# Performance work log

Hardware: AMD Instinct MI355X
Metric: run time of the kernel (lower is better)

The kernel has to match this reference:

```python
import jax, jax.numpy as jnp
import numpy as np

NUM_HEADS = 16
NUM_KV_GROUPS = 4
EPS = 1e-6


def _rms_norm(x, w):
    # normalize over last dim (head_dim)
    return x * jax.lax.rsqrt(jnp.mean(x * x, axis=-1, keepdims=True) + EPS) * w


def _rope_cos_sin(T, head_dim):
    half = head_dim // 2
    inv_freq = 1.0 / (10000.0 ** (jnp.arange(half, dtype=jnp.float32) / half))
    freqs = jnp.arange(T, dtype=jnp.float32)[:, None] * inv_freq[None, :]  # [T, half]
    cos = jnp.repeat(jnp.cos(freqs), 2, axis=-1)  # [T, head_dim]
    sin = jnp.repeat(jnp.sin(freqs), 2, axis=-1)
    return cos, sin


def _apply_rope(x, cos, sin):
    # x: [B, H, T, head_dim]; cos/sin broadcast over B,H
    x1 = x[..., ::2]
    x2 = x[..., 1::2]
    x_rot = jnp.stack([-x2, x1], axis=-1).reshape(x.shape)  # interleave (-x2, x1)
    return x * cos + x_rot * sin


def setup_inputs() -> dict:
    key = jax.random.key(0)
    ks = jax.random.split(key, 5)
    scale = lambda k, sh: jax.random.normal(k, sh, dtype=jnp.float32) * 0.02
    return {
        "x": jax.random.normal(ks[0], (4, 2048, 1024), dtype=jnp.float32),
        "Wq": scale(ks[1], (1024, 1024)),
        "Wk": scale(ks[2], (256, 1024)),
        "Wv": scale(ks[3], (256, 1024)),
        "Wo": scale(ks[4], (1024, 1024)),
        "qn_w": jnp.ones((64,), jnp.float32),
        "kn_w": jnp.ones((64,), jnp.float32),
    }


def reference(x, Wq, Wk, Wv, Wo, qn_w, kn_w):
    B, T, D = x.shape
    H, G = NUM_HEADS, NUM_KV_GROUPS
    hd = D // H

    # projections (torch Linear: y = x @ W.T), reshape to [B, heads, T, hd]
    q = (x @ Wq.T).reshape(B, T, H, hd).transpose(0, 2, 1, 3)
    k = (x @ Wk.T).reshape(B, T, G, hd).transpose(0, 2, 1, 3)
    v = (x @ Wv.T).reshape(B, T, G, hd).transpose(0, 2, 1, 3)

    # optional qk RMSNorm (qk_norm=True)
    q = _rms_norm(q, qn_w)
    k = _rms_norm(k, kn_w)

    # RoPE (position_offset = 0)
    cos, sin = _rope_cos_sin(T, hd)
    q = _apply_rope(q, cos, sin)
    k = _apply_rope(k, cos, sin)

    # GQA: expand kv heads to match query heads
    rep = H // G
    k = jnp.repeat(k, rep, axis=1)
    v = jnp.repeat(v, rep, axis=1)

    # causal SDPA
    scores = jnp.einsum('bhqd,bhkd->bhqk', q, k) / jnp.sqrt(jnp.float32(hd))
    causal = jnp.tril(jnp.ones((T, T), dtype=bool))
    scores = jnp.where(causal, scores, jnp.float32(-1e30))
    attn = jax.nn.softmax(scores, axis=-1)
    out = jnp.einsum('bhqk,bhkd->bhqd', attn, v)

    out = out.transpose(0, 2, 1, 3).reshape(B, T, D)
    return out @ Wo.T
```

## Files before the change

kernel.cpp:

```cpp
#include <hip/hip_runtime.h>

typedef unsigned short u16;
typedef __attribute__((ext_vector_type(8))) short bf16x8;
typedef __attribute__((ext_vector_type(4))) short bf16x4;
typedef __attribute__((ext_vector_type(4))) float f32x4;

#define GP(p) ((const __attribute__((address_space(1))) void*)(unsigned long long)(p))
#define LP(p) ((__attribute__((address_space(3))) void*)(unsigned int)(unsigned long long)(p))

#define QSCALE 0.180336879486998f

__device__ __forceinline__ u16 f2bf(float f) {
  union { float f; unsigned u; } v; v.f = f;
  unsigned r = v.u + 0x7fffu + ((v.u >> 16) & 1u);
  return (u16)(r >> 16);
}
__device__ __forceinline__ short f2bf_cvt(float f) {
  __bf16 b = (__bf16)f;
  return *reinterpret_cast<short*>(&b);
}

#if __has_builtin(__builtin_amdgcn_mfma_f32_16x16x16bf16_1k)
#define MFMA16(A, B, C) __builtin_amdgcn_mfma_f32_16x16x16bf16_1k((A), (B), (C), 0, 0, 0)
#elif __has_builtin(__builtin_amdgcn_mfma_f32_16x16x16_bf16)
#define MFMA16(A, B, C) __builtin_amdgcn_mfma_f32_16x16x16_bf16((A), (B), (C), 0, 0, 0)
#else
static __device__ __forceinline__ f32x4 mfma16_asm(bf16x4 a, bf16x4 b, f32x4 c) {
  asm volatile("v_mfma_f32_16x16x16_bf16 %0, %1, %2, %0" : "+v"(c) : "v"(a), "v"(b));
  return c;
}
#define MFMA16(A, B, C) mfma16_asm((A), (B), (C))
#endif

__global__ void prep_kernel(const float* __restrict__ x,
                            const float* __restrict__ Wq, const float* __restrict__ Wk,
                            const float* __restrict__ Wv, const float* __restrict__ Wo,
                            u16* __restrict__ xb, u16* __restrict__ Wcat,
                            u16* __restrict__ Wob,
                            float* __restrict__ ctab, float* __restrict__ stab) {
  const int bid = blockIdx.x, tid = threadIdx.x;
  if (bid < 2048) {
    for (int i = bid * 256 + tid; i < 2097152; i += 2048 * 256) {
      float4 v = reinterpret_cast<const float4*>(x)[i];
      reinterpret_cast<ushort4*>(xb)[i] =
          make_ushort4(f2bf(v.x), f2bf(v.y), f2bf(v.z), f2bf(v.w));
    }
  } else if (bid < 2688) {
    for (int i = (bid - 2048) * 256 + tid; i < 655360; i += 640 * 256) {
      const float* src; u16* dst; int off;
      if (i < 262144)      { src = Wq; dst = Wcat;           off = i; }
      else if (i < 327680) { src = Wk; dst = Wcat + 1048576; off = i - 262144; }
      else if (i < 393216) { src = Wv; dst = Wcat + 1310720; off = i - 327680; }
      else                 { src = Wo; dst = Wob;            off = i - 393216; }
      float4 v = reinterpret_cast<const float4*>(src)[off];
      reinterpret_cast<ushort4*>(dst)[off] =
          make_ushort4(f2bf(v.x), f2bf(v.y), f2bf(v.z), f2bf(v.w));
    }
  } else {
    int i = (bid - 2688) * 256 + tid;
    int t = i >> 5, f = i & 31;
    float inv = exp2f((float)f * (-13.287712379549449f / 32.0f));
    float ang = (float)t * inv;
    float sv, cv;
    sincosf(ang, &sv, &cv);
    ctab[i] = cv;
    stab[i] = sv;
  }
}

__launch_bounds__(256)
__global__ void gemm_qkv_kernel(const u16* __restrict__ A, const u16* __restrict__ W,
                                u16* __restrict__ qh, u16* __restrict__ kh,
                                u16* __restrict__ vt,
                                const float* __restrict__ qn_w, const float* __restrict__ kn_w,
                                const float* __restrict__ ctab, const float* __restrict__ stab) {
  __shared__ __align__(16) u16 As[2][128 * 64];
  __shared__ __align__(16) u16 Bs[2][128 * 64];
  const int tid = threadIdx.x;
  const int w = tid >> 6, l = tid & 63;
  const int lr = l & 15, lk = l >> 4;
  const int wr = w >> 1, wc = w & 1;
  const int m0 = blockIdx.x * 128, n0 = blockIdx.y * 128;
  const u16* ap[4];
  const u16* bp[4];
#pragma unroll
  for (int i = 0; i < 4; ++i) {
    int c = i * 256 + tid;
    ap[i] = A + (size_t)(m0 + (c >> 3)) * 1024 + (c & 7) * 8;
    bp[i] = W + (size_t)(n0 + (c >> 3)) * 1024 + (c & 7) * 8;
  }
  auto stage = [&](int buf) {
#pragma unroll
    for (int i = 0; i < 4; ++i) {
      __builtin_amdgcn_global_load_lds(GP(ap[i]),
          LP((char*)&As[0][0] + buf * 16384 + (i * 256 + (tid & ~63)) * 16), 16, 0, 0);
      __builtin_amdgcn_global_load_lds(GP(bp[i]),
          LP((char*)&Bs[0][0] + buf * 16384 + (i * 256 + (tid & ~63)) * 16), 16, 0, 0);
      ap[i] += 64; bp[i] += 64;
    }
  };
  f32x4 acc[4][4] = {};
  int cur = 0;
  stage(0);
  asm volatile("s_waitcnt vmcnt(0)" ::: "memory");
  __builtin_amdgcn_s_barrier();
  for (int k0 = 0; k0 < 1024; k0 += 64) {
    if (k0 < 960) stage(cur ^ 1);
    __builtin_amdgcn_s_setprio(1);
#pragma unroll
    for (int kk = 0; kk < 2; ++kk) {
      bf16x8 af[4], bfr[4];
#pragma unroll
      for (int fi = 0; fi < 4; ++fi)
        af[fi] = *reinterpret_cast<const bf16x8*>(
            &As[cur][(wr * 64 + fi * 16 + lr) * 64 + kk * 32 + lk * 8]);
#pragma unroll
      for (int fj = 0; fj < 4; ++fj)
        bfr[fj] = *reinterpret_cast<const bf16x8*>(
            &Bs[cur][(wc * 64 + fj * 16 + lr) * 64 + kk * 32 + lk * 8]);
#pragma unroll
      for (int fi = 0; fi < 4; ++fi)
#pragma unroll
        for (int fj = 0; fj < 4; ++fj)
          acc[fi][fj] = __builtin_amdgcn_mfma_f32_16x16x32_bf16(af[fi], bfr[fj], acc[fi][fj], 0, 0, 0);
    }
    __builtin_amdgcn_s_setprio(0);
    asm volatile("s_waitcnt vmcnt(0)" ::: "memory");
    __builtin_amdgcn_s_barrier();
    cur ^= 1;
  }
  const int ncol0 = n0 + wc * 64;
  if (ncol0 < 1280) {
    const bool isq = ncol0 < 1024;
    const float* wn = isq ? qn_w : kn_w;
    const float sc = isq ? QSCALE : 1.0f;
    float wv[4];
#pragma unroll
    for (int fj = 0; fj < 4; ++fj) wv[fj] = wn[fj * 16 + lr];
#pragma unroll
    for (int fi = 0; fi < 4; ++fi)
#pragma unroll
      for (int r = 0; r < 4; ++r) {
        float ss = 0.f;
#pragma unroll
        for (int fj = 0; fj < 4; ++fj) ss += acc[fi][fj][r] * acc[fi][fj][r];
        ss += __shfl_xor(ss, 1); ss += __shfl_xor(ss, 2);
        ss += __shfl_xor(ss, 4); ss += __shfl_xor(ss, 8);
        float rinv = rsqrtf(ss * (1.0f / 64.0f) + 1e-6f);
        int m = m0 + wr * 64 + fi * 16 + lk * 4 + r;
        int t = m & 2047, b = m >> 11;
#pragma unroll
        for (int fj = 0; fj < 4; ++fj) {
          float xn = acc[fi][fj][r] * rinv * wv[fj];
          float pr = __shfl_xor(xn, 1);
          float rot = (lr & 1) ? pr : -pr;
          int ci = t * 32 + fj * 8 + (lr >> 1);
          u16 outv = f2bf((xn * ctab[ci] + rot * stab[ci]) * sc);
          int n = ncol0 + fj * 16 + lr;
          if (isq) {
            int h = n >> 6, d = n & 63;
            qh[((size_t)((b * 16 + h) * 2048 + t)) * 64 + d] = outv;
          } else {
            int n2 = n - 1024, g = n2 >> 6, d = n2 & 63;
            kh[((size_t)((b * 4 + g) * 2048 + t)) * 64 + d] = outv;
          }
        }
      }
  } else {
#pragma unroll
    for (int fi = 0; fi < 4; ++fi)
#pragma unroll
      for (int fj = 0; fj < 4; ++fj) {
        int m = m0 + wr * 64 + fi * 16 + lk * 4;
        int b = m >> 11, t = m & 2047;
        int n2 = ncol0 + fj * 16 + lr - 1280;
        int g = n2 >> 6, d = n2 & 63;
        bf16x4 o;
#pragma unroll
        for (int r = 0; r < 4; ++r) o[r] = f2bf_cvt(acc[fi][fj][r]);
        *reinterpret_cast<bf16x4*>(&vt[((size_t)((b * 4 + g) * 64 + d)) * 2048 + t]) = o;
      }
  }
}

__launch_bounds__(512)
__global__ void attn_kernel(const u16* __restrict__ qh, const u16* __restrict__ kh,
                            const u16* __restrict__ vt, u16* __restrict__ ao) {
  __shared__ __align__(16) u16 Ks[2][64 * 64];
  __shared__ __align__(16) u16 Vts[2][64 * 64];
  const int tid = threadIdx.x, w = tid >> 6, l = tid & 63;
  const int lr = l & 15, lk = l >> 4;
  const int wq = w & 3, wh = w >> 2;
  const int D = blockIdx.x;
  const int j = D >> 3;
  const int p = j & 15, hp = (j >> 4) & 1;
  const int z = (D & 7) + 8 * (j >> 5);
  const int b = z >> 2, g = z & 3;
  const int h = g * 4 + hp * 2 + wh;
  const u16* Qh = qh + ((size_t)((b * 16 + h) * 2048)) * 64;
  const u16* Kb = kh + ((size_t)z * 2048) * 64;
  const u16* Vtb = vt + ((size_t)z * 64) * 2048;
  const int swz = (lr & 7) * 8;

  const int r0 = tid >> 3, s0 = ((tid & 7) ^ (r0 & 7)) * 8;
  char* kd = (char*)&Ks[0][0] + (tid & ~63) * 16;
  char* vd = (char*)&Vts[0][0] + (tid & ~63) * 16;
  const u16* kp; const u16* vp;

  auto stage = [&](int buf) {
    __builtin_amdgcn_global_load_lds(GP(kp), LP(kd + buf * 8192), 16, 0, 0);
    __builtin_amdgcn_global_load_lds(GP(vp), LP(vd + buf * 8192), 16, 0, 0);
    kp += 64 * 64; vp += 64;
  };

  const u16* kbase[2];
  kbase[0] = &Ks[0][lr * 64 + ((lk * 8) ^ swz)];
  kbase[1] = &Ks[0][lr * 64 + ((32 + lk * 8) ^ swz)];
  const u16* vbase[4];
#pragma unroll
  for (int fi = 0; fi < 4; ++fi)
    vbase[fi] = &Vts[0][lr * 64 + ((fi * 16 + lk * 4) ^ swz)];

  auto run_qtile = [&](int qt) {
    const int q0 = qt * 64;
    const u16* Qb = Qh + (size_t)(q0 + wq * 16) * 64;
    const bf16x8 qf0 = *reinterpret_cast<const bf16x8*>(&Qb[lr * 64 + lk * 8]);
    const bf16x8 qf1 = *reinterpret_cast<const bf16x8*>(&Qb[lr * 64 + 32 + lk * 8]);
    f32x4 oacc[4] = {};
    float lrow = 0.f;
    kp = Kb + r0 * 64 + s0;
    vp = Vtb + (size_t)r0 * 2048 + s0;
    stage(0);
    asm volatile("s_waitcnt vmcnt(0)" ::: "memory");
    __builtin_amdgcn_s_barrier();

    auto round = [&](int it, int buf) {
      if (it < qt) stage(buf ^ 1);
      f32x4 sacc[4] = {};
      __builtin_amdgcn_s_setprio(1);
#pragma unroll
      for (int kk = 0; kk < 2; ++kk) {
        bf16x8 qf = kk ? qf1 : qf0;
#pragma unroll
        for (int fi = 0; fi < 4; ++fi) {
          bf16x8 kf = *reinterpret_cast<const bf16x8*>(kbase[kk] + buf * 4096 + fi * 1024);
          sacc[fi] = __builtin_amdgcn_mfma_f32_16x16x32_bf16(kf, qf, sacc[fi], 0, 0, 0);
        }
      }
      __builtin_amdgcn_s_setprio(0);
      if (it == qt) {
        int qloc = wq * 16 + lr;
#pragma unroll
        for (int fi = 0; fi < 4; ++fi)
#pragma unroll
          for (int r = 0; r < 4; ++r)
            if (fi * 16 + lk * 4 + r > qloc) sacc[fi][r] = -1e30f;
      }
      bf16x4 pb[4];
#pragma unroll
      for (int fi = 0; fi < 4; ++fi)
#pragma unroll
        for (int r = 0; r < 4; ++r) {
          float pv = exp2f(sacc[fi][r]);
          lrow += pv;
          pb[fi][r] = f2bf_cvt(pv);
        }
      __builtin_amdgcn_s_setprio(1);
#pragma unroll
      for (int fi = 0; fi < 4; ++fi)
#pragma unroll
        for (int db = 0; db < 4; ++db) {
          bf16x4 vf = *reinterpret_cast<const bf16x4*>(vbase[fi] + buf * 4096 + db * 1024);
          oacc[db] = MFMA16(vf, pb[fi], oacc[db]);
        }
      __builtin_amdgcn_s_setprio(0);
      asm volatile("s_waitcnt vmcnt(0)" ::: "memory");
      __builtin_amdgcn_s_barrier();
    };

    const int nIt = qt + 1;
    for (int it = 0; it < nIt; it += 2) {
      round(it, 0);
      if (it + 1 < nIt) round(it + 1, 1);
    }

    float lsum = lrow;
    lsum += __shfl_xor(lsum, 16);
    lsum += __shfl_xor(lsum, 32);
    float inv = 1.0f / lsum;
#pragma unroll
    for (int db = 0; db < 4; ++db) {
      bf16x4 o;
#pragma unroll
      for (int r = 0; r < 4; ++r) o[r] = f2bf_cvt(oacc[db][r] * inv);
      *reinterpret_cast<bf16x4*>(
          &ao[((size_t)(b * 2048 + q0 + wq * 16 + lr)) * 1024 + h * 64 + db * 16 + lk * 4]) = o;
    }
  };
  run_qtile(31 - p);
  run_qtile(p);
}

__launch_bounds__(256)
__global__ void gemm_out_kernel(const u16* __restrict__ A, const u16* __restrict__ W,
                                float* __restrict__ out) {
  __shared__ __align__(16) u16 As[2][128 * 64];
  __shared__ __align__(16) u16 Bs[2][128 * 64];
  const int tid = threadIdx.x;
  const int w = tid >> 6, l = tid & 63;
  const int lr = l & 15, lk = l >> 4;
  const int wr = w >> 1, wc = w & 1;
  const int bid = blockIdx.x;
  const int m0 = (bid >> 3) * 128, n0 = (bid & 7) * 128;
  const u16* ap[4];
  const u16* bp[4];
#pragma unroll
  for (int i = 0; i < 4; ++i) {
    int c = i * 256 + tid;
    ap[i] = A + (size_t)(m0 + (c >> 3)) * 1024 + (c & 7) * 8;
    bp[i] = W + (size_t)(n0 + (c >> 3)) * 1024 + (c & 7) * 8;
  }
  auto stage = [&](int buf) {
#pragma unroll
    for (int i = 0; i < 4; ++i) {
      __builtin_amdgcn_global_load_lds(GP(ap[i]),
          LP((char*)&As[0][0] + buf * 16384 + (i * 256 + (tid & ~63)) * 16), 16, 0, 0);
      __builtin_amdgcn_global_load_lds(GP(bp[i]),
          LP((char*)&Bs[0][0] + buf * 16384 + (i * 256 + (tid & ~63)) * 16), 16, 0, 0);
      ap[i] += 64; bp[i] += 64;
    }
  };
  f32x4 acc[4][4] = {};
  int cur = 0;
  stage(0);
  asm volatile("s_waitcnt vmcnt(0)" ::: "memory");
  __builtin_amdgcn_s_barrier();
  for (int k0 = 0; k0 < 1024; k0 += 64) {
    if (k0 < 960) stage(cur ^ 1);
    __builtin_amdgcn_s_setprio(1);
#pragma unroll
    for (int kk = 0; kk < 2; ++kk) {
      bf16x8 af[4], bfr[4];
#pragma unroll
      for (int fi = 0; fi < 4; ++fi)
        af[fi] = *reinterpret_cast<const bf16x8*>(
            &As[cur][(wr * 64 + fi * 16 + lr) * 64 + kk * 32 + lk * 8]);
#pragma unroll
      for (int fj = 0; fj < 4; ++fj)
        bfr[fj] = *reinterpret_cast<const bf16x8*>(
            &Bs[cur][(wc * 64 + fj * 16 + lr) * 64 + kk * 32 + lk * 8]);
#pragma unroll
      for (int fi = 0; fi < 4; ++fi)
#pragma unroll
        for (int fj = 0; fj < 4; ++fj)
          acc[fi][fj] = __builtin_amdgcn_mfma_f32_16x16x32_bf16(af[fi], bfr[fj], acc[fi][fj], 0, 0, 0);
    }
    __builtin_amdgcn_s_setprio(0);
    asm volatile("s_waitcnt vmcnt(0)" ::: "memory");
    __builtin_amdgcn_s_barrier();
    cur ^= 1;
  }
#pragma unroll
  for (int fi = 0; fi < 4; ++fi)
#pragma unroll
    for (int fj = 0; fj < 4; ++fj)
#pragma unroll
      for (int r = 0; r < 4; ++r) {
        int m = m0 + wr * 64 + fi * 16 + lk * 4 + r;
        int n = n0 + wc * 64 + fj * 16 + lr;
        out[(size_t)m * 1024 + n] = acc[fi][fj][r];
      }
}

extern "C" void kernel_launch(void* const* d_in, const int* in_sizes, int n_in,
                              void* d_out, int out_size, void* d_ws, size_t ws_size,
                              hipStream_t stream) {
  const float* x  = (const float*)d_in[0];
  const float* Wq = (const float*)d_in[1];
  const float* Wk = (const float*)d_in[2];
  const float* Wv = (const float*)d_in[3];
  const float* Wo = (const float*)d_in[4];
  const float* qn = (const float*)d_in[5];
  const float* kn = (const float*)d_in[6];
  float* out = (float*)d_out;
  char* ws = (char*)d_ws;
  u16* xb   = (u16*)(ws);
  u16* Wcat = (u16*)(ws + 16777216);
  u16* Wob  = (u16*)(ws + 19922944);
  u16* qh   = (u16*)(ws + 22020096);
  u16* kh   = (u16*)(ws + 38797312);
  u16* vtb  = (u16*)(ws + 42991616);
  u16* ao   = (u16*)(ws + 47185920);
  float* ctab = (float*)ao;
  float* stab = ctab + 65536;

  prep_kernel<<<2944, 256, 0, stream>>>(x, Wq, Wk, Wv, Wo, xb, Wcat, Wob, ctab, stab);
  dim3 g1(64, 12);
  gemm_qkv_kernel<<<g1, 256, 0, stream>>>(xb, Wcat, qh, kh, vtb, qn, kn, ctab, stab);
  attn_kernel<<<512, 512, 0, stream>>>(qh, kh, vtb, ao);
  gemm_out_kernel<<<512, 256, 0, stream>>>(ao, Wob, out);
}
```

Measured before the change: 155.6 us.

## Split long causal q-tiles across block pairs with partial-result merge via atomics

Each attention block now handles two query heads sharing the same KV group, so every K/V tile loaded into LDS feeds both heads. The long-tile key range is split between two blocks: one does the first 17 KV tiles and the other does the rest plus the short tile. Partial outputs and row sums go to workspace, and the second block to finish, detected with an atomic flag, merges and normalizes them. Row sums are now computed with an MFMA against a ones vector, and the launch-bounds hint changes. This is meant to balance causal work across blocks and reuse K/V, at the cost of more registers, extra partial traffic through global memory, and a bf16 rounding of the partial accumulators.

```diff
diff --git a/kernel.cpp b/kernel.cpp
--- a/kernel.cpp
+++ b/kernel.cpp
@@ -18,6 +18,10 @@
 __device__ __forceinline__ short f2bf_cvt(float f) {
   __bf16 b = (__bf16)f;
   return *reinterpret_cast<short*>(&b);
+}
+__device__ __forceinline__ float bf2f(u16 u) {
+  union { unsigned u; float f; } v; v.u = ((unsigned)u) << 16;
+  return v.f;
 }
 
 #if __has_builtin(__builtin_amdgcn_mfma_f32_16x16x16bf16_1k)
@@ -37,7 +41,8 @@
                             const float* __restrict__ Wv, const float* __restrict__ Wo,
                             u16* __restrict__ xb, u16* __restrict__ Wcat,
                             u16* __restrict__ Wob,
-                            float* __restrict__ ctab, float* __restrict__ stab) {
+                            float* __restrict__ ctab, float* __restrict__ stab,
+                            int* __restrict__ flags) {
   const int bid = blockIdx.x, tid = threadIdx.x;
   if (bid < 2048) {
     for (int i = bid * 256 + tid; i < 2097152; i += 2048 * 256) {
@@ -56,7 +61,7 @@
       reinterpret_cast<ushort4*>(dst)[off] =
           make_ushort4(f2bf(v.x), f2bf(v.y), f2bf(v.z), f2bf(v.w));
     }
-  } else {
+  } else if (bid < 2944) {
     int i = (bid - 2688) * 256 + tid;
     int t = i >> 5, f = i & 31;
     float inv = exp2f((float)f * (-13.287712379549449f / 32.0f));
@@ -65,6 +70,8 @@
     sincosf(ang, &sv, &cv);
     ctab[i] = cv;
     stab[i] = sv;
+  } else {
+    if (tid < 240) flags[tid] = 0;
   }
 }
 
@@ -183,24 +190,30 @@
   }
 }
 
-__launch_bounds__(512)
+__launch_bounds__(512, 4)
 __global__ void attn_kernel(const u16* __restrict__ qh, const u16* __restrict__ kh,
-                            const u16* __restrict__ vt, u16* __restrict__ ao) {
+                            const u16* __restrict__ vt, u16* __restrict__ ao,
+                            u16* __restrict__ part, float* __restrict__ plsum,
+                            int* __restrict__ flags) {
   __shared__ __align__(16) u16 Ks[2][64 * 64];
   __shared__ __align__(16) u16 Vts[2][64 * 64];
+  __shared__ int sOld;
   const int tid = threadIdx.x, w = tid >> 6, l = tid & 63;
   const int lr = l & 15, lk = l >> 4;
   const int wq = w & 3, wh = w >> 2;
   const int D = blockIdx.x;
   const int j = D >> 3;
-  const int p = j & 15, hp = (j >> 4) & 1;
+  const int p = j & 15, half = (j >> 4) & 1;
   const int z = (D & 7) + 8 * (j >> 5);
   const int b = z >> 2, g = z & 3;
-  const int h = g * 4 + hp * 2 + wh;
-  const u16* Qh = qh + ((size_t)((b * 16 + h) * 2048)) * 64;
+  const int h0 = g * 4 + wh * 2;
+  const u16* Qh0 = qh + ((size_t)((b * 16 + h0) * 2048)) * 64;
+  const u16* Qh1 = qh + ((size_t)((b * 16 + h0 + 1) * 2048)) * 64;
   const u16* Kb = kh + ((size_t)z * 2048) * 64;
   const u16* Vtb = vt + ((size_t)z * 64) * 2048;
   const int swz = (lr & 7) * 8;
+  const int qtA = 31 - p, qtB = p;
+  const int tile = z * 15 + p;
 
   const int r0 = tid >> 3, s0 = ((tid & 7) ^ (r0 & 7)) * 8;
   char* kd = (char*)&Ks[0][0] + (tid & ~63) * 16;
@@ -221,30 +234,37 @@
   for (int fi = 0; fi < 4; ++fi)
     vbase[fi] = &Vts[0][lr * 64 + ((fi * 16 + lk * 4) ^ swz)];
 
-  auto run_qtile = [&](int qt) {
+  bf16x4 ones;
+#pragma unroll
+  for (int r = 0; r < 4; ++r) ones[r] = (short)0x3F80;
+
+  auto run_seg = [&](int qt, int it0, int it1, bool complete) {
     const int q0 = qt * 64;
-    const u16* Qb = Qh + (size_t)(q0 + wq * 16) * 64;
-    const bf16x8 qf0 = *reinterpret_cast<const bf16x8*>(&Qb[lr * 64 + lk * 8]);
-    const bf16x8 qf1 = *reinterpret_cast<const bf16x8*>(&Qb[lr * 64 + 32 + lk * 8]);
-    f32x4 oacc[4] = {};
-    float lrow = 0.f;
-    kp = Kb + r0 * 64 + s0;
-    vp = Vtb + (size_t)r0 * 2048 + s0;
+    const u16* QA = Qh0 + (size_t)(q0 + wq * 16) * 64;
+    const u16* QB = Qh1 + (size_t)(q0 + wq * 16) * 64;
+    const bf16x8 qA0 = *reinterpret_cast<const bf16x8*>(&QA[lr * 64 + lk * 8]);
+    const bf16x8 qA1 = *reinterpret_cast<const bf16x8*>(&QA[lr * 64 + 32 + lk * 8]);
+    const bf16x8 qB0 = *reinterpret_cast<const bf16x8*>(&QB[lr * 64 + lk * 8]);
+    const bf16x8 qB1 = *reinterpret_cast<const bf16x8*>(&QB[lr * 64 + 32 + lk * 8]);
+    f32x4 oacc0[4] = {}, oacc1[4] = {};
+    f32x4 lacc0 = {}, lacc1 = {};
+    kp = Kb + (size_t)it0 * 4096 + r0 * 64 + s0;
+    vp = Vtb + (size_t)r0 * 2048 + it0 * 64 + s0;
     stage(0);
     asm volatile("s_waitcnt vmcnt(0)" ::: "memory");
     __builtin_amdgcn_s_barrier();
 
     auto round = [&](int it, int buf) {
-      if (it < qt) stage(buf ^ 1);
-      f32x4 sacc[4] = {};
+      if (it + 1 < it1) stage(buf ^ 1);
+      f32x4 s0a[4] = {}, s1a[4] = {};
       __builtin_amdgcn_s_setprio(1);
 #pragma unroll
       for (int kk = 0; kk < 2; ++kk) {
-        bf16x8 qf = kk ? qf1 : qf0;
 #pragma unroll
         for (int fi = 0; fi < 4; ++fi) {
           bf16x8 kf = *reinterpret_cast<const bf16x8*>(kbase[kk] + buf * 4096 + fi * 1024);
-          sacc[fi] = __builtin_amdgcn_mfma_f32_16x16x32_bf16(kf, qf, sacc[fi], 0, 0, 0);
+          s0a[fi] = __builtin_amdgcn_mfma_f32_16x16x32_bf16(kf, kk ? qA1 : qA0, s0a[fi], 0, 0, 0);
+          s1a[fi] = __builtin_amdgcn_mfma_f32_16x16x32_bf16(kf, kk ? qB1 : qB0, s1a[fi], 0, 0, 0);
         }
       }
       __builtin_amdgcn_s_setprio(0);
@@ -254,51 +274,105 @@
         for (int fi = 0; fi < 4; ++fi)
 #pragma unroll
           for (int r = 0; r < 4; ++r)
-            if (fi * 16 + lk * 4 + r > qloc) sacc[fi][r] = -1e30f;
-      }
-      bf16x4 pb[4];
+            if (fi * 16 + lk * 4 + r > qloc) { s0a[fi][r] = -1e30f; s1a[fi][r] = -1e30f; }
+      }
+      bf16x4 pb0[4], pb1[4];
 #pragma unroll
       for (int fi = 0; fi < 4; ++fi)
 #pragma unroll
         for (int r = 0; r < 4; ++r) {
-          float pv = exp2f(sacc[fi][r]);
-          lrow += pv;
-          pb[fi][r] = f2bf_cvt(pv);
+          pb0[fi][r] = f2bf_cvt(exp2f(s0a[fi][r]));
+          pb1[fi][r] = f2bf_cvt(exp2f(s1a[fi][r]));
         }
       __builtin_amdgcn_s_setprio(1);
+#pragma unroll
+      for (int fi = 0; fi < 4; ++fi) {
+        lacc0 = MFMA16(ones, pb0[fi], lacc0);
+        lacc1 = MFMA16(ones, pb1[fi], lacc1);
+      }
 #pragma unroll
       for (int fi = 0; fi < 4; ++fi)
 #pragma unroll
         for (int db = 0; db < 4; ++db) {
           bf16x4 vf = *reinterpret_cast<const bf16x4*>(vbase[fi] + buf * 4096 + db * 1024);
-          oacc[db] = MFMA16(vf, pb[fi], oacc[db]);
+          oacc0[db] = MFMA16(vf, pb0[fi], oacc0[db]);
+          oacc1[db] = MFMA16(vf, pb1[fi], oacc1[db]);
         }
       __builtin_amdgcn_s_setprio(0);
       asm volatile("s_waitcnt vmcnt(0)" ::: "memory");
       __builtin_amdgcn_s_barrier();
     };
-
-    const int nIt = qt + 1;
-    for (int it = 0; it < nIt; it += 2) {
+    for (int it = it0; it < it1; it += 2) {
       round(it, 0);
-      if (it + 1 < nIt) round(it + 1, 1);
-    }
-
-    float lsum = lrow;
-    lsum += __shfl_xor(lsum, 16);
-    lsum += __shfl_xor(lsum, 32);
-    float inv = 1.0f / lsum;
-#pragma unroll
-    for (int db = 0; db < 4; ++db) {
-      bf16x4 o;
-#pragma unroll
-      for (int r = 0; r < 4; ++r) o[r] = f2bf_cvt(oacc[db][r] * inv);
-      *reinterpret_cast<bf16x4*>(
-          &ao[((size_t)(b * 2048 + q0 + wq * 16 + lr)) * 1024 + h * 64 + db * 16 + lk * 4]) = o;
+      if (it + 1 < it1) round(it + 1, 1);
+    }
+
+    const int qrow = wq * 16 + lr;
+    if (complete) {
+#pragma unroll
+      for (int hh = 0; hh < 2; ++hh) {
+        const f32x4* oacc = hh ? oacc1 : oacc0;
+        float inv = 1.0f / (hh ? lacc1[0] : lacc0[0]);
+#pragma unroll
+        for (int db = 0; db < 4; ++db) {
+          bf16x4 o;
+#pragma unroll
+          for (int r = 0; r < 4; ++r) o[r] = f2bf_cvt(oacc[db][r] * inv);
+          *reinterpret_cast<bf16x4*>(
+              &ao[((size_t)(b * 2048 + q0 + qrow)) * 1024 + (h0 + hh) * 64 + db * 16 + lk * 4]) = o;
+        }
+      }
+    } else {
+#pragma unroll
+      for (int hh = 0; hh < 2; ++hh) {
+        const f32x4* oacc = hh ? oacc1 : oacc0;
+        float ls = hh ? lacc1[0] : lacc0[0];
+        size_t pbase = ((size_t)(tile * 2 + half) * 4 + wh * 2 + hh) * 4096;
+#pragma unroll
+        for (int db = 0; db < 4; ++db) {
+          bf16x4 o;
+#pragma unroll
+          for (int r = 0; r < 4; ++r) o[r] = f2bf_cvt(oacc[db][r]);
+          *reinterpret_cast<bf16x4*>(&part[pbase + qrow * 64 + db * 16 + lk * 4]) = o;
+        }
+        if (lk == 0)
+          plsum[((size_t)(tile * 2 + half) * 4 + wh * 2 + hh) * 64 + qrow] = ls;
+      }
+      __syncthreads();
+      __threadfence();
+      if (tid == 0) sOld = atomicAdd(&flags[tile], 1);
+      __syncthreads();
+      if (sOld == 1) {
+        __threadfence();
+        const int oh = half ^ 1;
+#pragma unroll
+        for (int hh = 0; hh < 2; ++hh) {
+          const f32x4* oacc = hh ? oacc1 : oacc0;
+          float ls = hh ? lacc1[0] : lacc0[0];
+          size_t obase = ((size_t)(tile * 2 + oh) * 4 + wh * 2 + hh) * 4096;
+          float lo = plsum[((size_t)(tile * 2 + oh) * 4 + wh * 2 + hh) * 64 + qrow];
+          float inv = 1.0f / (ls + lo);
+#pragma unroll
+          for (int db = 0; db < 4; ++db) {
+            bf16x4 of = *reinterpret_cast<const bf16x4*>(&part[obase + qrow * 64 + db * 16 + lk * 4]);
+            bf16x4 o;
+#pragma unroll
+            for (int r = 0; r < 4; ++r)
+              o[r] = f2bf_cvt((oacc[db][r] + bf2f((u16)of[r])) * inv);
+            *reinterpret_cast<bf16x4*>(
+                &ao[((size_t)(b * 2048 + q0 + qrow)) * 1024 + (h0 + hh) * 64 + db * 16 + lk * 4]) = o;
+          }
+        }
+      }
     }
   };
-  run_qtile(31 - p);
-  run_qtile(p);
+
+  if (half == 0) {
+    run_seg(qtA, 0, 17, p == 15);
+  } else {
+    if (p < 15) run_seg(qtA, 17, qtA + 1, false);
+    run_seg(qtB, 0, qtB + 1, true);
+  }
 }
 
 __launch_bounds__(256)
@@ -393,10 +467,13 @@
   u16* ao   = (u16*)(ws + 47185920);
   float* ctab = (float*)ao;
   float* stab = ctab + 65536;
-
-  prep_kernel<<<2944, 256, 0, stream>>>(x, Wq, Wk, Wv, Wo, xb, Wcat, Wob, ctab, stab);
+  u16* part    = (u16*)(ws);
+  float* plsum = (float*)(ws + 15728640);
+  int* flags   = (int*)(ws + 63963136);
+
+  prep_kernel<<<2945, 256, 0, stream>>>(x, Wq, Wk, Wv, Wo, xb, Wcat, Wob, ctab, stab, flags);
   dim3 g1(64, 12);
   gemm_qkv_kernel<<<g1, 256, 0, stream>>>(xb, Wcat, qh, kh, vtb, qn, kn, ctab, stab);
-  attn_kernel<<<512, 512, 0, stream>>>(qh, kh, vtb, ao);
+  attn_kernel<<<512, 512, 0, stream>>>(qh, kh, vtb, ao, part, plsum, flags);
   gemm_out_kernel<<<512, 256, 0, stream>>>(ao, Wob, out);
 }
```

Measured after the change: 321.1 us. 2.06x slower.
